# Kernel tuning notes

Hardware: AMD Instinct MI355X
Metric: run time of the kernel (lower is better)

The kernel has to match this reference:

```python
import jax, jax.numpy as jnp
import numpy as np
from jax import lax

DEPTH = 2
HEADS = 8
TEMP = 1.0

def _ln_last(x, g, b, eps=1e-5):
    m = x.mean(-1, keepdims=True)
    v = ((x - m) ** 2).mean(-1, keepdims=True)
    return (x - m) / jnp.sqrt(v + eps) * g + b

def _ln_chan(x, g, b, eps=1e-6):
    # torch custom LayerNorm over channel dim of NCHW, biased var
    m = x.mean(1, keepdims=True)
    v = ((x - m) ** 2).mean(1, keepdims=True)
    return (x - m) / jnp.sqrt(v + eps) * g[None, :, None, None] + b[None, :, None, None]

def _conv3x3(x, w):
    return lax.conv_general_dilated(x, w, (1, 1), ((1, 1), (1, 1)),
                                    dimension_numbers=('NCHW', 'OIHW', 'NCHW'))

def _transformer(x, ln1_g, ln1_b, qkv_w, qkv_b, out_w, out_b, ln2_g, ln2_b,
                 mlp_w1, mlp_b1, mlp_w2, mlp_b2):
    dim = x.shape[-1]
    dh = dim // HEADS
    scale = dh ** -0.5
    for i in range(DEPTH):
        h = _ln_last(x, ln1_g[i], ln1_b[i])
        qkv = h @ qkv_w[i] + qkv_b[i]
        q, k, v = jnp.split(qkv, 3, axis=-1)
        sp = lambda t: t.reshape(t.shape[0], t.shape[1], HEADS, dh).transpose(0, 2, 1, 3)
        q, k, v = sp(q), sp(k), sp(v)
        attn = jax.nn.softmax(jnp.einsum('bhid,bhjd->bhij', q, k) * scale, axis=-1) / TEMP
        o = jnp.einsum('bhij,bhjd->bhid', attn, v).transpose(0, 2, 1, 3).reshape(x.shape)
        x = o @ out_w[i] + out_b[i] + x
        h = _ln_last(x, ln2_g[i], ln2_b[i])
        x = jax.nn.gelu(h @ mlp_w1[i] + mlp_b1[i], approximate=False) @ mlp_w2[i] + mlp_b2[i] + x
    return x

def _tacf(support_feature, query_feature, task_descriptor, ln1_g, ln1_b, qkv_w, qkv_b,
          out_w, out_b, ln2_g, ln2_b, mlp_w1, mlp_b1, mlp_w2, mlp_b2,
          rfm_ln_g, rfm_ln_b, rfm_conv1, rfm_conv2, rfm_conv3, rfm_conv4):
    n, c, h, w = support_feature.shape
    M = task_descriptor.shape[1]
    # descriptor generator: 'n c h w -> 1 (n h w) c', prepend descriptors
    sf = support_feature.transpose(0, 2, 3, 1).reshape(1, n * h * w, c)
    x = jnp.concatenate([task_descriptor, sf], axis=1)
    x = _transformer(x, ln1_g, ln1_b, qkv_w, qkv_b, out_w, out_b, ln2_g, ln2_b,
                     mlp_w1, mlp_b1, mlp_w2, mlp_b2)
    key0 = x[0, :M, :]  # (M, C)

    def region(feat):
        # mean over C of feat[:,None,c,h,w]*key[m,c] == matmul / C
        return jax.nn.sigmoid(jnp.einsum('bchw,mc->bmhw', feat, key0) / feat.shape[1])

    def map_fuse(reg, feat):
        # mean over m of (feat*task + feat) == feat*(mean_m(task)+1)
        return feat * (reg.mean(1, keepdims=True) + 1.0)

    def rfm(x4):
        t = _ln_chan(x4, rfm_ln_g, rfm_ln_b)
        t = jax.nn.relu(_conv3x3(t, rfm_conv1))
        t = jax.nn.relu(_conv3x3(t, rfm_conv2))
        t = jax.nn.relu(_conv3x3(t, rfm_conv3))
        t = _conv3x3(t, rfm_conv4)
        b_, T_, h_, w_ = t.shape
        t = jax.nn.sigmoid(t.reshape(b_, T_, h_ * w_))  # (B,T,HW)
        feat = x4.transpose(0, 2, 3, 1).reshape(b_, h_ * w_, -1)  # (B,HW,C)
        out = jnp.einsum('btp,bpc->btc', t, feat) / (h_ * w_)  # mean over HW
        return out.transpose(0, 2, 1)  # (B,C,T)

    qr = region(query_feature)
    sr = region(support_feature)
    aq = map_fuse(qr, query_feature)
    asp = map_fuse(sr, support_feature)
    return (rfm(asp), rfm(aq))

def setup_inputs() -> dict:
    key = jax.random.key(0)
    ks = jax.random.split(key, 12)
    B_S, B_Q, C, H, W = 25, 75, 128, 10, 10
    M, T, MLP = 16, 32, 512
    rn = lambda k, s, sc=1.0: jax.random.normal(k, s, dtype=jnp.float32) * sc
    return {
        'support_feature': rn(ks[0], (B_S, C, H, W)),
        'query_feature': rn(ks[1], (B_Q, C, H, W)),
        'task_descriptor': rn(ks[2], (1, M, C)),
        'ln1_g': jnp.ones((DEPTH, C), jnp.float32), 'ln1_b': jnp.zeros((DEPTH, C), jnp.float32),
        'qkv_w': rn(ks[3], (DEPTH, C, 3 * C), 0.02), 'qkv_b': jnp.zeros((DEPTH, 3 * C), jnp.float32),
        'out_w': rn(ks[4], (DEPTH, C, C), 0.02), 'out_b': jnp.zeros((DEPTH, C), jnp.float32),
        'ln2_g': jnp.ones((DEPTH, C), jnp.float32), 'ln2_b': jnp.zeros((DEPTH, C), jnp.float32),
        'mlp_w1': rn(ks[5], (DEPTH, C, MLP), 0.02), 'mlp_b1': jnp.zeros((DEPTH, MLP), jnp.float32),
        'mlp_w2': rn(ks[6], (DEPTH, MLP, C), 0.02), 'mlp_b2': jnp.zeros((DEPTH, C), jnp.float32),
        'rfm_ln_g': jnp.ones((C,), jnp.float32), 'rfm_ln_b': jnp.zeros((C,), jnp.float32),
        'rfm_conv1': rn(ks[7], (T, C, 3, 3), 0.05),
        'rfm_conv2': rn(ks[8], (T, T, 3, 3), 0.05),
        'rfm_conv3': rn(ks[9], (T, T, 3, 3), 0.05),
        'rfm_conv4': rn(ks[10], (T, T, 3, 3), 0.05),
    }

def reference(support_feature, query_feature, task_descriptor, ln1_g, ln1_b, qkv_w, qkv_b,
              out_w, out_b, ln2_g, ln2_b, mlp_w1, mlp_b1, mlp_w2, mlp_b2,
              rfm_ln_g, rfm_ln_b, rfm_conv1, rfm_conv2, rfm_conv3, rfm_conv4):
    return _tacf(support_feature, query_feature, task_descriptor, ln1_g, ln1_b, qkv_w, qkv_b,
                 out_w, out_b, ln2_g, ln2_b, mlp_w1, mlp_b1, mlp_w2, mlp_b2,
                 rfm_ln_g, rfm_ln_b, rfm_conv1, rfm_conv2, rfm_conv3, rfm_conv4)
```

## Files before the change

kernel.cpp:

```cpp
#include <hip/hip_runtime.h>
#include <math.h>

#define SEQ 2516
#define SEQP 2520
#define SEQP2 2560
#define CDIM 128

typedef __attribute__((ext_vector_type(8))) short short8;
typedef __attribute__((ext_vector_type(4))) float f32x4;

__device__ __forceinline__ float gelu_exact(float x) {
    return x * 0.5f * (1.0f + erff(x * 0.7071067811865475f));
}
__device__ __forceinline__ float fexp2(float x) { return __builtin_amdgcn_exp2f(x); }
__device__ __forceinline__ short f2bf(float f) {
    unsigned u = __float_as_uint(f);
    unsigned r = 0x7fffu + ((u >> 16) & 1u);
    return (short)((u + r) >> 16);
}
__device__ __forceinline__ short f2bf_trunc(float f) {
    return (short)(__float_as_uint(f) >> 16);
}

__global__ __launch_bounds__(64) void concat_ln_kernel(
    const float* __restrict__ td, const float* __restrict__ sup,
    const float* __restrict__ g, const float* __restrict__ b,
    float* __restrict__ X, float* __restrict__ H) {
    const int row = blockIdx.x;
    const int t = threadIdx.x;
    float x0, x1;
    if (row < 16) {
        x0 = td[row * 128 + t];
        x1 = td[row * 128 + 64 + t];
    } else {
        int r = row - 16;
        int n = r / 100, p = r - n * 100;
        x0 = sup[n * 12800 + t * 100 + p];
        x1 = sup[n * 12800 + (t + 64) * 100 + p];
    }
    X[row * 128 + t] = x0;
    X[row * 128 + 64 + t] = x1;
    float s = x0 + x1;
    for (int off = 32; off > 0; off >>= 1) s += __shfl_down(s, off);
    float mean = __shfl(s, 0) * (1.f / 128.f);
    float d0 = x0 - mean, d1 = x1 - mean;
    float v = d0 * d0 + d1 * d1;
    for (int off = 32; off > 0; off >>= 1) v += __shfl_down(v, off);
    float var = __shfl(v, 0) * (1.f / 128.f);
    float rstd = rsqrtf(var + 1e-5f);
    H[row * 128 + t]      = d0 * rstd * g[t] + b[t];
    H[row * 128 + 64 + t] = d1 * rstd * g[t + 64] + b[t + 64];
}

__global__ __launch_bounds__(256) void qkv_mfma_kernel(
    const float* __restrict__ A, const float* __restrict__ W,
    const float* __restrict__ bias,
    short* __restrict__ Qbf, short* __restrict__ Kbf, short* __restrict__ VTb,
    int q_mt) {
    if (blockIdx.y < 2 && (int)blockIdx.x >= q_mt) return;
    __shared__ __align__(16) short Wt[64 * 136];
    const int t = threadIdx.x;
    const int wave = t >> 6, lane = t & 63;
    const int quad = lane >> 4, c16 = lane & 15;
    const int m0 = blockIdx.x * 64;
    const int n0 = blockIdx.y * 64;
    const float SC = 0.25f * 1.4426950408889634f;
    #pragma unroll
    for (int pass = 0; pass < 4; ++pass) {
        int idx = t + pass * 256;
        int n = idx & 63, kc = idx >> 6;
        short8 wv;
        #pragma unroll
        for (int j = 0; j < 8; ++j)
            wv[j] = f2bf(W[(size_t)(kc * 8 + j) * 384 + n0 + n]);
        *(short8*)&Wt[n * 136 + kc * 8] = wv;
    }
    __syncthreads();
    const int am = m0 + wave * 16 + c16;
    f32x4 acc[4];
    #pragma unroll
    for (int i = 0; i < 4; ++i) acc[i] = (f32x4){0.f, 0.f, 0.f, 0.f};
    #pragma unroll
    for (int kk = 0; kk < 4; ++kk) {
        const float4* ap = (const float4*)(A + (size_t)am * 128 + kk * 32 + quad * 8);
        float4 a0 = ap[0], a1 = ap[1];
        short8 af;
        af[0] = f2bf(a0.x); af[1] = f2bf(a0.y); af[2] = f2bf(a0.z); af[3] = f2bf(a0.w);
        af[4] = f2bf(a1.x); af[5] = f2bf(a1.y); af[6] = f2bf(a1.z); af[7] = f2bf(a1.w);
        #pragma unroll
        for (int ns = 0; ns < 4; ++ns) {
            short8 wf = *(const short8*)&Wt[(ns * 16 + c16) * 136 + kk * 32 + quad * 8];
            acc[ns] = __builtin_amdgcn_mfma_f32_16x16x32_bf16(af, wf, acc[ns], 0, 0, 0);
        }
    }
    const int region = __builtin_amdgcn_readfirstlane(n0 >> 7);
    #pragma unroll
    for (int ns = 0; ns < 4; ++ns) {
        const int n = n0 + ns * 16 + c16;
        float bv = bias[n];
        #pragma unroll
        for (int r = 0; r < 4; ++r) {
            const int row = m0 + wave * 16 + quad * 4 + r;
            float v = acc[ns][r] + bv;
            if (region == 0)      Qbf[(size_t)row * 128 + n] = f2bf(v * SC);
            else if (region == 1) Kbf[(size_t)row * 128 + (n - 128)] = f2bf(v);
            else                  VTb[(size_t)(n - 256) * SEQP2 + row] = f2bf(v);
        }
    }
}

__global__ __launch_bounds__(256) void mlp_fused_kernel(
    const float* __restrict__ A, const float* __restrict__ W1,
    const float* __restrict__ b1, const float* __restrict__ W2,
    float* __restrict__ PARTG) {
    __shared__ __align__(16) short W1t[64 * 136];
    __shared__ __align__(16) short W2t[128 * 72];
    __shared__ __align__(16) short Ct[4 * 16 * 72];
    const int t = threadIdx.x;
    const int wave = t >> 6, lane = t & 63;
    const int quad = lane >> 4, c16 = lane & 15;
    const int m0 = blockIdx.x * 64;
    const int kz = blockIdx.y;
    const int n0 = kz * 64;
    #pragma unroll
    for (int pass = 0; pass < 4; ++pass) {
        int idx = t + pass * 256;
        int n = idx & 63, kc = idx >> 6;
        short8 wv;
        #pragma unroll
        for (int j = 0; j < 8; ++j)
            wv[j] = f2bf(W1[(size_t)(kc * 8 + j) * 512 + n0 + n]);
        *(short8*)&W1t[n * 136 + kc * 8] = wv;
    }
    {
        const int n = t & 127, half = t >> 7;
        #pragma unroll
        for (int c = 0; c < 4; ++c) {
            short8 wv;
            #pragma unroll
            for (int j = 0; j < 8; ++j)
                wv[j] = f2bf(W2[(size_t)(n0 + half * 32 + c * 8 + j) * 128 + n]);
            *(short8*)&W2t[n * 72 + half * 32 + c * 8] = wv;
        }
    }
    __syncthreads();
    const int am = m0 + wave * 16 + c16;
    f32x4 acc1[4];
    #pragma unroll
    for (int i = 0; i < 4; ++i) acc1[i] = (f32x4){0.f, 0.f, 0.f, 0.f};
    #pragma unroll
    for (int kk = 0; kk < 4; ++kk) {
        const float4* ap = (const float4*)(A + (size_t)am * 128 + kk * 32 + quad * 8);
        float4 a0 = ap[0], a1 = ap[1];
        short8 af;
        af[0] = f2bf(a0.x); af[1] = f2bf(a0.y); af[2] = f2bf(a0.z); af[3] = f2bf(a0.w);
        af[4] = f2bf(a1.x); af[5] = f2bf(a1.y); af[6] = f2bf(a1.z); af[7] = f2bf(a1.w);
        #pragma unroll
        for (int ns = 0; ns < 4; ++ns) {
            short8 wf = *(const short8*)&W1t[(ns * 16 + c16) * 136 + kk * 32 + quad * 8];
            acc1[ns] = __builtin_amdgcn_mfma_f32_16x16x32_bf16(af, wf, acc1[ns], 0, 0, 0);
        }
    }
    short* Cw = Ct + wave * 16 * 72;
    #pragma unroll
    for (int ns = 0; ns < 4; ++ns) {
        float bv = b1[n0 + ns * 16 + c16];
        #pragma unroll
        for (int r = 0; r < 4; ++r)
            Cw[(quad * 4 + r) * 72 + ns * 16 + c16] = f2bf(gelu_exact(acc1[ns][r] + bv));
    }
    f32x4 acc2[8];
    #pragma unroll
    for (int i = 0; i < 8; ++i) acc2[i] = (f32x4){0.f, 0.f, 0.f, 0.f};
    #pragma unroll
    for (int kk = 0; kk < 2; ++kk) {
        short8 af2 = *(const short8*)&Cw[c16 * 72 + kk * 32 + quad * 8];
        #pragma unroll
        for (int ns = 0; ns < 8; ++ns) {
            short8 wf = *(const short8*)&W2t[(ns * 16 + c16) * 72 + kk * 32 + quad * 8];
            acc2[ns] = __builtin_amdgcn_mfma_f32_16x16x32_bf16(af2, wf, acc2[ns], 0, 0, 0);
        }
    }
    float* dst = PARTG + (size_t)kz * SEQP2 * 128;
    #pragma unroll
    for (int ns = 0; ns < 8; ++ns) {
        #pragma unroll
        for (int r = 0; r < 4; ++r) {
            const int row = m0 + wave * 16 + quad * 4 + r;
            dst[(size_t)row * 128 + ns * 16 + c16] = acc2[ns][r];
        }
    }
}

__global__ __launch_bounds__(512) void combine_ln_kernel(
    const float* __restrict__ PARTG, const float* __restrict__ bias,
    const float* __restrict__ R, float* __restrict__ C, float* __restrict__ H,
    const float* __restrict__ g, const float* __restrict__ bb, int M) {
    __shared__ float ln[8][130];
    const int t = threadIdx.x;
    const int c = t & 127;
    const int grp = __builtin_amdgcn_readfirstlane(t >> 7);
    const int r0 = blockIdx.x * 8 + grp * 2;
    #pragma unroll
    for (int i = 0; i < 2; ++i) {
        const int row = r0 + i;
        float v = bias[c] + R[(size_t)row * 128 + c];
        #pragma unroll
        for (int kz = 0; kz < 8; ++kz)
            v += PARTG[(size_t)kz * SEQP2 * 128 + (size_t)row * 128 + c];
        ln[grp * 2 + i][c] = v;
        if (row < M) C[(size_t)row * 128 + c] = v;
    }
    __syncthreads();
    const int wv = t >> 6, l = t & 63;
    float x0 = ln[wv][l], x1 = ln[wv][l + 64];
    float s = x0 + x1;
    for (int off = 32; off > 0; off >>= 1) s += __shfl_down(s, off);
    float mean = __shfl(s, 0) * (1.f / 128.f);
    float d0 = x0 - mean, d1 = x1 - mean;
    float vv = d0 * d0 + d1 * d1;
    for (int off = 32; off > 0; off >>= 1) vv += __shfl_down(vv, off);
    float var = __shfl(vv, 0) * (1.f / 128.f);
    float rstd = rsqrtf(var + 1e-5f);
    const int hrow = blockIdx.x * 8 + wv;
    H[(size_t)hrow * 128 + l]      = d0 * rstd * g[l] + bb[l];
    H[(size_t)hrow * 128 + 64 + l] = d1 * rstd * g[l + 64] + bb[l + 64];
}

__global__ __launch_bounds__(512) void proj_merge_ln_kernel(
    const float* __restrict__ PART, const float* __restrict__ W,
    const float* __restrict__ bias, const float* __restrict__ R,
    float* __restrict__ C, float* __restrict__ H,
    const float* __restrict__ g, const float* __restrict__ bb, int M) {
    __shared__ float ln[8][130];
    const int t = threadIdx.x;
    const int c = t & 127;
    const int grp = __builtin_amdgcn_readfirstlane(t >> 7);
    const int r0 = blockIdx.x * 8 + grp * 2;
    float acc0 = 0.f, acc1 = 0.f;
    #pragma unroll
    for (int h = 0; h < 8; ++h) {
        const float* p0a = PART + ((size_t)h * SEQP + r0) * 20;
        const float* p1a = PART + ((size_t)(8 + h) * SEQP + r0) * 20;
        const float* p0b = p0a + 20;
        const float* p1b = p1a + 20;
        float m0 = p0a[16], l0 = p0a[17], m1 = p1a[16], l1 = p1a[17];
        float Ma = fmaxf(m0, m1);
        float w0 = fexp2(m0 - Ma), w1 = fexp2(m1 - Ma);
        float inva = 1.f / fmaf(l0, w0, l1 * w1);
        float c0a = w0 * inva, c1a = w1 * inva;
        m0 = p0b[16]; l0 = p0b[17]; m1 = p1b[16]; l1 = p1b[17];
        float Mb = fmaxf(m0, m1);
        w0 = fexp2(m0 - Mb); w1 = fexp2(m1 - Mb);
        float invb = 1.f / fmaf(l0, w0, l1 * w1);
        float c0b = w0 * invb, c1b = w1 * invb;
        #pragma unroll
        for (int kk = 0; kk < 4; ++kk) {
            const int k0 = h * 16 + kk * 4;
            float w_0 = W[(size_t)(k0 + 0) * 128 + c];
            float w_1 = W[(size_t)(k0 + 1) * 128 + c];
            float w_2 = W[(size_t)(k0 + 2) * 128 + c];
            float w_3 = W[(size_t)(k0 + 3) * 128 + c];
            float4 x0 = *(const float4*)&p0a[kk * 4];
            float4 y0 = *(const float4*)&p1a[kk * 4];
            float4 x1 = *(const float4*)&p0b[kk * 4];
            float4 y1 = *(const float4*)&p1b[kk * 4];
            float a00 = x0.x * c0a + y0.x * c1a;
            float a01 = x0.y * c0a + y0.y * c1a;
            float a02 = x0.z * c0a + y0.z * c1a;
            float a03 = x0.w * c0a + y0.w * c1a;
            float a10 = x1.x * c0b + y1.x * c1b;
            float a11 = x1.y * c0b + y1.y * c1b;
            float a12 = x1.z * c0b + y1.z * c1b;
            float a13 = x1.w * c0b + y1.w * c1b;
            acc0 = fmaf(a00, w_0, acc0); acc0 = fmaf(a01, w_1, acc0);
            acc0 = fmaf(a02, w_2, acc0); acc0 = fmaf(a03, w_3, acc0);
            acc1 = fmaf(a10, w_0, acc1); acc1 = fmaf(a11, w_1, acc1);
            acc1 = fmaf(a12, w_2, acc1); acc1 = fmaf(a13, w_3, acc1);
        }
    }
    float bv = bias[c];
    float v0 = acc0 + bv + R[(size_t)(r0 + 0) * 128 + c];
    float v1 = acc1 + bv + R[(size_t)(r0 + 1) * 128 + c];
    ln[grp * 2 + 0][c] = v0;
    ln[grp * 2 + 1][c] = v1;
    if (r0 + 0 < M) C[(size_t)(r0 + 0) * 128 + c] = v0;
    if (r0 + 1 < M) C[(size_t)(r0 + 1) * 128 + c] = v1;
    __syncthreads();
    const int wv = t >> 6, l = t & 63;
    float x0 = ln[wv][l], x1 = ln[wv][l + 64];
    float s = x0 + x1;
    for (int off = 32; off > 0; off >>= 1) s += __shfl_down(s, off);
    float mean = __shfl(s, 0) * (1.f / 128.f);
    float d0 = x0 - mean, d1 = x1 - mean;
    float vv = d0 * d0 + d1 * d1;
    for (int off = 32; off > 0; off >>= 1) vv += __shfl_down(vv, off);
    float var = __shfl(vv, 0) * (1.f / 128.f);
    float rstd = rsqrtf(var + 1e-5f);
    const int hrow = blockIdx.x * 8 + wv;
    H[(size_t)hrow * 128 + l]      = d0 * rstd * g[l] + bb[l];
    H[(size_t)hrow * 128 + 64 + l] = d1 * rstd * g[l + 64] + bb[l + 64];
}

__global__ __launch_bounds__(128) void attn_kernel(
    const short* __restrict__ Qbf, const short* __restrict__ Kbf,
    const short* __restrict__ VTb, float* __restrict__ PART) {
    __shared__ __align__(16) short sKs[9600];
    short* Ks = sKs;
    short* Vt = sKs + 3072;
    const int t = threadIdx.x;
    const int wave = t >> 6, lane = t & 63;
    const int quad = lane >> 4, c16 = lane & 15;
    short* Pw = sKs + 3072 + 2176 + wave * 16 * 136;
    const int head = blockIdx.y, z = blockIdx.z;
    const int qb = blockIdx.x * 32 + wave * 16;

    short8 qf;
    #pragma unroll
    for (int i = 0; i < 8; ++i) qf[i] = 0;
    if (quad < 2)
        qf = *(const short8*)(Qbf + (size_t)(qb + c16) * 128 + head * 16 + quad * 8);
    f32x4 oacc = {0.f, 0.f, 0.f, 0.f};
    float m_[4] = {-INFINITY, -INFINITY, -INFINITY, -INFINITY};
    float l_[4] = {0.f, 0.f, 0.f, 0.f};

    const int vdim = t >> 3, vseg = t & 7;
    const int tA = z * 10, tB = z ? 20 : 10;
    for (int ti = tA; ti < tB; ++ti) {
        const int tile0 = ti * 128;
        if (ti != tA) __syncthreads();
        {
            const short8* kp = (const short8*)(Kbf + (size_t)(tile0 + t) * 128 + head * 16);
            *(short8*)&Ks[t * 24]     = kp[0];
            *(short8*)&Ks[t * 24 + 8] = kp[1];
            const short8* vp = (const short8*)(VTb + (size_t)(head * 16 + vdim) * SEQP2 + tile0 + vseg * 16);
            *(short8*)&Vt[vdim * 136 + vseg * 16]     = vp[0];
            *(short8*)&Vt[vdim * 136 + vseg * 16 + 8] = vp[1];
        }
        __syncthreads();

        f32x4 sA[4], sB[4];
        #pragma unroll
        for (int st = 0; st < 4; ++st) {
            const int k0 = st * 32;
            short8 kfA, kfB;
            #pragma unroll
            for (int i = 0; i < 8; ++i) { kfA[i] = 0; kfB[i] = 0; }
            if (quad < 2) {
                kfA = *(const short8*)&Ks[(k0 + c16) * 24 + quad * 8];
                kfB = *(const short8*)&Ks[(k0 + 16 + c16) * 24 + quad * 8];
            }
            f32x4 zz = {0.f, 0.f, 0.f, 0.f};
            sA[st] = __builtin_amdgcn_mfma_f32_16x16x32_bf16(qf, kfA, zz, 0, 0, 0);
            sB[st] = __builtin_amdgcn_mfma_f32_16x16x32_bf16(qf, kfB, zz, 0, 0, 0);
            const bool badA = (tile0 + k0 + c16) >= SEQ;
            const bool badB = (tile0 + k0 + 16 + c16) >= SEQ;
            if (badA) { sA[st][0] = -1e30f; sA[st][1] = -1e30f; sA[st][2] = -1e30f; sA[st][3] = -1e30f; }
            if (badB) { sB[st][0] = -1e30f; sB[st][1] = -1e30f; sB[st][2] = -1e30f; sB[st][3] = -1e30f; }
        }
        #pragma unroll
        for (int r = 0; r < 4; ++r) {
            float v = fmaxf(sA[0][r], sB[0][r]);
            #pragma unroll
            for (int st = 1; st < 4; ++st) v = fmaxf(v, fmaxf(sA[st][r], sB[st][r]));
            v = fmaxf(v, __shfl_xor(v, 1));
            v = fmaxf(v, __shfl_xor(v, 2));
            v = fmaxf(v, __shfl_xor(v, 4));
            v = fmaxf(v, __shfl_xor(v, 8));
            float nm = fmaxf(m_[r], v);
            float corr = fexp2(m_[r] - nm);
            m_[r] = nm;
            oacc[r] *= corr;
            l_[r] *= corr;
        }
        #pragma unroll
        for (int st = 0; st < 4; ++st) {
            #pragma unroll
            for (int r = 0; r < 4; ++r) {
                float eA = fexp2(sA[st][r] - m_[r]);
                float eB = fexp2(sB[st][r] - m_[r]);
                l_[r] += eA + eB;
                Pw[(quad * 4 + r) * 136 + st * 32 + c16]      = f2bf_trunc(eA);
                Pw[(quad * 4 + r) * 136 + st * 32 + 16 + c16] = f2bf_trunc(eB);
            }
        }
        #pragma unroll
        for (int st = 0; st < 4; ++st) {
            short8 pf = *(const short8*)&Pw[c16 * 136 + st * 32 + quad * 8];
            short8 vf = *(const short8*)&Vt[c16 * 136 + st * 32 + quad * 8];
            oacc = __builtin_amdgcn_mfma_f32_16x16x32_bf16(pf, vf, oacc, 0, 0, 0);
        }
    }
    #pragma unroll
    for (int r = 0; r < 4; ++r) {
        float lr = l_[r];
        lr += __shfl_xor(lr, 1);
        lr += __shfl_xor(lr, 2);
        lr += __shfl_xor(lr, 4);
        lr += __shfl_xor(lr, 8);
        const int qrow = qb + quad * 4 + r;
        if (qrow < SEQ) {
            float* dst = PART + ((size_t)(z * 8 + head) * SEQP + qrow) * 20;
            dst[c16] = oacc[r];
            if (c16 == 0) { dst[16] = m_[r]; dst[17] = lr; }
        }
    }
}

__global__ __launch_bounds__(256) void region_fuse_stats_kernel(
    const float* __restrict__ sup, const float* __restrict__ qry,
    const float* __restrict__ X, float* __restrict__ fused,
    float* __restrict__ MEAN, float* __restrict__ RSTD) {
    __shared__ float key0[2048];
    __shared__ float rfac[100];
    const int b = blockIdx.x;
    const int t = threadIdx.x;
    const float* feat = (b < 25) ? (sup + (size_t)b * 12800) : (qry + (size_t)(b - 25) * 12800);
    for (int i = t; i < 2048; i += 256) key0[i] = X[i];
    __syncthreads();
    if (t < 100) {
        float dots[16];
        #pragma unroll
        for (int mm = 0; mm < 16; ++mm) dots[mm] = 0.f;
        float s = 0.f, ss = 0.f;
        for (int c = 0; c < 128; ++c) {
            float f = feat[c * 100 + t];
            s += f; ss += f * f;
            #pragma unroll
            for (int mm = 0; mm < 16; ++mm) dots[mm] += f * key0[mm * 128 + c];
        }
        float mean16 = 0.f;
        #pragma unroll
        for (int mm = 0; mm < 16; ++mm) mean16 += 1.f / (1.f + expf(-dots[mm] * (1.f / 128.f)));
        float r = mean16 * (1.f / 16.f) + 1.f;
        rfac[t] = r;
        float mr = s * (1.f / 128.f);
        float vr = ss * (1.f / 128.f) - mr * mr;
        MEAN[b * 128 + t] = mr * r;
        RSTD[b * 128 + t] = rsqrtf(vr * r * r + 1e-6f);
    }
    __syncthreads();
    for (int i = t; i < 12800; i += 256)
        fused[(size_t)b * 12800 + i] = feat[i] * rfac[i % 100];
}

__global__ __launch_bounds__(256) void conv1_split_kernel(
    const float* __restrict__ in, const float* __restrict__ w,
    const float* __restrict__ MEAN, const float* __restrict__ RSTD,
    const float* __restrict__ g, const float* __restrict__ bb,
    float* __restrict__ PARTC) {
    __shared__ float sin_[32 * 144];
    const int b = blockIdx.x;
    const int base_to = blockIdx.y * 8;
    const int cb = blockIdx.z * 32;
    const int t = threadIdx.x;
    const int h = __builtin_amdgcn_readfirstlane(t >> 7);
    const int p = t & 127;
    const int py = p / 10, px = p - py * 10;
    const bool active = p < 100;
    float acc[4] = {0.f, 0.f, 0.f, 0.f};
    for (int i = t; i < 32 * 144; i += 256) {
        int c = i / 144, pos = i - c * 144;
        int y = pos / 12 - 1, x = pos % 12 - 1;
        float v = 0.f;
        if ((unsigned)y < 10u && (unsigned)x < 10u) {
            int pp = y * 10 + x;
            float raw = in[(size_t)b * 12800 + (cb + c) * 100 + pp];
            v = (raw - MEAN[b * 128 + pp]) * RSTD[b * 128 + pp] * g[cb + c] + bb[cb + c];
        }
        sin_[i] = v;
    }
    __syncthreads();
    if (active) {
        const float* wbase = w + ((size_t)(base_to + h * 4) * 128 + cb) * 9;
        for (int c = 0; c < 32; ++c) {
            const float* sp = &sin_[c * 144 + py * 12 + px];
            float pix[9];
            #pragma unroll
            for (int k = 0; k < 9; ++k) pix[k] = sp[(k / 3) * 12 + (k % 3)];
            #pragma unroll
            for (int j = 0; j < 4; ++j) {
                const float* wq = wbase + ((size_t)j * 128 + c) * 9;
                #pragma unroll
                for (int k = 0; k < 9; ++k) acc[j] = fmaf(pix[k], wq[k], acc[j]);
            }
        }
        #pragma unroll
        for (int j = 0; j < 4; ++j)
            PARTC[((size_t)blockIdx.z * 100 + b) * 3200 + (base_to + h * 4 + j) * 100 + p] = acc[j];
    }
}

template<bool RELU, bool COMBINE>
__global__ __launch_bounds__(256) void conv3x3_to4_kernel(
    const float* __restrict__ in, const float* __restrict__ w,
    float* __restrict__ out) {
    __shared__ float sin_[32 * 144];
    const int b = blockIdx.x;
    const int base_to = blockIdx.y * 4;
    const int t = threadIdx.x;
    const int h = __builtin_amdgcn_readfirstlane(t >> 7);
    const int p = t & 127;
    const int py = p / 10, px = p - py * 10;
    const bool active = p < 100;
    float acc[2] = {0.f, 0.f};
    for (int i = t; i < 32 * 144; i += 256) {
        int c = i / 144, pos = i - c * 144;
        int y = pos / 12 - 1, x = pos % 12 - 1;
        float v = 0.f;
        if ((unsigned)y < 10u && (unsigned)x < 10u) {
            if (COMBINE) {
                const size_t base = (size_t)b * 3200 + c * 100 + y * 10 + x;
                v = in[base] + in[base + 320000] + in[base + 640000] + in[base + 960000];
                v = fmaxf(v, 0.f);
            } else {
                v = in[(size_t)b * 3200 + c * 100 + y * 10 + x];
            }
        }
        sin_[i] = v;
    }
    __syncthreads();
    if (active) {
        const float* wbase = w + ((size_t)(base_to + h * 2) * 32) * 9;
        for (int c = 0; c < 32; ++c) {
            const float* sp = &sin_[c * 144 + py * 12 + px];
            float pix[9];
            #pragma unroll
            for (int k = 0; k < 9; ++k) pix[k] = sp[(k / 3) * 12 + (k % 3)];
            #pragma unroll
            for (int j = 0; j < 2; ++j) {
                const float* wq = wbase + ((size_t)j * 32 + c) * 9;
                #pragma unroll
                for (int k = 0; k < 9; ++k) acc[j] = fmaf(pix[k], wq[k], acc[j]);
            }
        }
        #pragma unroll
        for (int j = 0; j < 2; ++j) {
            float v = acc[j];
            if (RELU) v = fmaxf(v, 0.f);
            out[(size_t)b * 3200 + (base_to + h * 2 + j) * 100 + p] = v;
        }
    }
}

__global__ __launch_bounds__(256) void conv4_rfm_kernel(
    const float* __restrict__ in, const float* __restrict__ w,
    const float* __restrict__ fused, float* __restrict__ out) {
    __shared__ float sin_[32 * 144];
    __shared__ float sig[4][104];
    const int b = blockIdx.x;
    const int base_to = blockIdx.y * 4;
    const int t = threadIdx.x;
    const int h = __builtin_amdgcn_readfirstlane(t >> 7);
    const int p = t & 127;
    const int py = p / 10, px = p - py * 10;
    const bool active = p < 100;
    float acc[2] = {0.f, 0.f};
    for (int i = t; i < 32 * 144; i += 256) {
        int c = i / 144, pos = i - c * 144;
        int y = pos / 12 - 1, x = pos % 12 - 1;
        float v = 0.f;
        if ((unsigned)y < 10u && (unsigned)x < 10u)
            v = in[(size_t)b * 3200 + c * 100 + y * 10 + x];
        sin_[i] = v;
    }
    __syncthreads();
    if (active) {
        const float* wbase = w + ((size_t)(base_to + h * 2) * 32) * 9;
        for (int c = 0; c < 32; ++c) {
            const float* sp = &sin_[c * 144 + py * 12 + px];
            float pix[9];
            #pragma unroll
            for (int k = 0; k < 9; ++k) pix[k] = sp[(k / 3) * 12 + (k % 3)];
            #pragma unroll
            for (int j = 0; j < 2; ++j) {
                const float* wq = wbase + ((size_t)j * 32 + c) * 9;
                #pragma unroll
                for (int k = 0; k < 9; ++k) acc[j] = fmaf(pix[k], wq[k], acc[j]);
            }
        }
        sig[h * 2 + 0][p] = 1.f / (1.f + expf(-acc[0]));
        sig[h * 2 + 1][p] = 1.f / (1.f + expf(-acc[1]));
    }
    __syncthreads();
    #pragma unroll
    for (int rep = 0; rep < 2; ++rep) {
        const int o = t + rep * 256;
        const int cc = o >> 2, ttl = o & 3;
        const float* fp = fused + (size_t)b * 12800 + cc * 100;
        float s = 0.f;
        for (int pp = 0; pp < 100; pp += 4) {
            float4 f4 = *(const float4*)&fp[pp];
            s += sig[ttl][pp] * f4.x + sig[ttl][pp + 1] * f4.y
               + sig[ttl][pp + 2] * f4.z + sig[ttl][pp + 3] * f4.w;
        }
        out[(size_t)b * 4096 + cc * 32 + base_to + ttl] = s * 0.01f;
    }
}

extern "C" void kernel_launch(void* const* d_in, const int* in_sizes, int n_in,
                              void* d_out, int out_size, void* d_ws, size_t ws_size,
                              hipStream_t stream) {
    (void)in_sizes; (void)n_in; (void)out_size; (void)ws_size;
    const float* sup    = (const float*)d_in[0];
    const float* qry    = (const float*)d_in[1];
    const float* td     = (const float*)d_in[2];
    const float* ln1_g  = (const float*)d_in[3];
    const float* ln1_b  = (const float*)d_in[4];
    const float* qkv_w  = (const float*)d_in[5];
    const float* qkv_b  = (const float*)d_in[6];
    const float* out_w  = (const float*)d_in[7];
    const float* out_b  = (const float*)d_in[8];
    const float* ln2_g  = (const float*)d_in[9];
    const float* ln2_b  = (const float*)d_in[10];
    const float* mlp_w1 = (const float*)d_in[11];
    const float* mlp_b1 = (const float*)d_in[12];
    const float* mlp_w2 = (const float*)d_in[13];
    const float* mlp_b2 = (const float*)d_in[14];
    const float* rg     = (const float*)d_in[15];
    const float* rb     = (const float*)d_in[16];
    const float* c1     = (const float*)d_in[17];
    const float* c2     = (const float*)d_in[18];
    const float* c3     = (const float*)d_in[19];
    const float* c4     = (const float*)d_in[20];
    float* out = (float*)d_out;

    float* ws   = (float*)d_ws;
    float* X    = ws;
    float* H    = X + 327680;
    float* PARTC= H + 327680;
    float* FUSED= PARTC + 1280000;
    float* MEAN = FUSED + 1280000;
    float* RSTD = MEAN + 12800;
    float* CB1  = RSTD + 12800;
    float* CB2  = CB1 + 320000;
    short* Qbf  = (short*)(CB2 + 320000);
    short* Kbf  = Qbf + 327680;
    short* VTb  = Kbf + 327680;
    float* PARTG= (float*)(VTb + 327680);
    float* PART = PARTG;

    const int SG = (SEQ + 7) / 8;
    const int MT = (SEQ + 63) / 64;

    concat_ln_kernel<<<SEQ, 64, 0, stream>>>(td, sup, ln1_g, ln1_b, X, H);
    for (int i = 0; i < 2; ++i) {
        const int qmt    = (i == 0) ? MT : 1;
        const int atiles = (i == 0) ? (SEQ + 31) / 32 : 1;
        const int sg     = (i == 0) ? SG : 2;
        const int mmt    = (i == 0) ? MT : 1;
        qkv_mfma_kernel<<<dim3(MT, 6), 256, 0, stream>>>(
            H, qkv_w + (size_t)i * 128 * 384, qkv_b + i * 384, Qbf, Kbf, VTb, qmt);
        attn_kernel<<<dim3(atiles, 8, 2), 128, 0, stream>>>(Qbf, Kbf, VTb, PART);
        proj_merge_ln_kernel<<<sg, 512, 0, stream>>>(
            PART, out_w + (size_t)i * 128 * 128, out_b + i * 128, X, X, H,
            ln2_g + i * 128, ln2_b + i * 128, SEQ);
        mlp_fused_kernel<<<dim3(mmt, 8), 256, 0, stream>>>(
            H, mlp_w1 + (size_t)i * 128 * 512, mlp_b1 + i * 512,
            mlp_w2 + (size_t)i * 512 * 128, PARTG);
        const float* ng = (i == 0) ? ln1_g + 128 : ln1_g;
        const float* nb = (i == 0) ? ln1_b + 128 : ln1_b;
        combine_ln_kernel<<<sg, 512, 0, stream>>>(
            PARTG, mlp_b2 + i * 128, X, X, H, ng, nb, SEQ);
    }
    region_fuse_stats_kernel<<<100, 256, 0, stream>>>(sup, qry, X, FUSED, MEAN, RSTD);
    conv1_split_kernel<<<dim3(100, 4, 4), 256, 0, stream>>>(FUSED, c1, MEAN, RSTD, rg, rb, PARTC);
    conv3x3_to4_kernel<true,  true ><<<dim3(100, 8), 256, 0, stream>>>(PARTC, c2, CB2);
    conv3x3_to4_kernel<true,  false><<<dim3(100, 8), 256, 0, stream>>>(CB2, c3, CB1);
    conv4_rfm_kernel<<<dim3(100, 8), 256, 0, stream>>>(CB1, c4, FUSED, out);
}
```

Baseline: 316.6 us.

## Rewrite RFM conv stack as bf16 MFMA implicit-GEMM kernels with channel-last layout

Replaces the scalar FP32 conv path (split-K conv1 with partial sums, per-output-group conv kernels, conv4 with reduction) with one block per sample that runs each 3x3 conv as an implicit GEMM on bf16 MFMA, using channel-last bf16 intermediates. The fused features are stored position-major (FUSEDT) so the final pooling reads coalesced columns. This removes the split-K partial buffers and the extra launches, and moves the conv FLOPs to matrix cores, at the cost of bf16 rounding of the activations and weights. The attention and MLP kernels only change position in the file.

New measurement: 274.6 us. -13.3%, faster.

```diff
diff --git a/kernel.cpp b/kernel.cpp
--- a/kernel.cpp
+++ b/kernel.cpp
@@ -109,122 +109,109 @@
     }
 }
 
-__global__ __launch_bounds__(256) void mlp_fused_kernel(
-    const float* __restrict__ A, const float* __restrict__ W1,
-    const float* __restrict__ b1, const float* __restrict__ W2,
-    float* __restrict__ PARTG) {
-    __shared__ __align__(16) short W1t[64 * 136];
-    __shared__ __align__(16) short W2t[128 * 72];
-    __shared__ __align__(16) short Ct[4 * 16 * 72];
+__global__ __launch_bounds__(128) void attn_kernel(
+    const short* __restrict__ Qbf, const short* __restrict__ Kbf,
+    const short* __restrict__ VTb, float* __restrict__ PART) {
+    __shared__ __align__(16) short sKs[9600];
+    short* Ks = sKs;
+    short* Vt = sKs + 3072;
     const int t = threadIdx.x;
     const int wave = t >> 6, lane = t & 63;
     const int quad = lane >> 4, c16 = lane & 15;
-    const int m0 = blockIdx.x * 64;
-    const int kz = blockIdx.y;
-    const int n0 = kz * 64;
-    #pragma unroll
-    for (int pass = 0; pass < 4; ++pass) {
-        int idx = t + pass * 256;
-        int n = idx & 63, kc = idx >> 6;
-        short8 wv;
-        #pragma unroll
-        for (int j = 0; j < 8; ++j)
-            wv[j] = f2bf(W1[(size_t)(kc * 8 + j) * 512 + n0 + n]);
-        *(short8*)&W1t[n * 136 + kc * 8] = wv;
-    }
-    {
-        const int n = t & 127, half = t >> 7;
-        #pragma unroll
-        for (int c = 0; c < 4; ++c) {
-            short8 wv;
-            #pragma unroll
-            for (int j = 0; j < 8; ++j)
-                wv[j] = f2bf(W2[(size_t)(n0 + half * 32 + c * 8 + j) * 128 + n]);
-            *(short8*)&W2t[n * 72 + half * 32 + c * 8] = wv;
-        }
-    }
-    __syncthreads();
-    const int am = m0 + wave * 16 + c16;
-    f32x4 acc1[4];
-    #pragma unroll
-    for (int i = 0; i < 4; ++i) acc1[i] = (f32x4){0.f, 0.f, 0.f, 0.f};
-    #pragma unroll
-    for (int kk = 0; kk < 4; ++kk) {
-        const float4* ap = (const float4*)(A + (size_t)am * 128 + kk * 32 + quad * 8);
-        float4 a0 = ap[0], a1 = ap[1];
-        short8 af;
-        af[0] = f2bf(a0.x); af[1] = f2bf(a0.y); af[2] = f2bf(a0.z); af[3] = f2bf(a0.w);
-        af[4] = f2bf(a1.x); af[5] = f2bf(a1.y); af[6] = f2bf(a1.z); af[7] = f2bf(a1.w);
-        #pragma unroll
-        for (int ns = 0; ns < 4; ++ns) {
-            short8 wf = *(const short8*)&W1t[(ns * 16 + c16) * 136 + kk * 32 + quad * 8];
-            acc1[ns] = __builtin_amdgcn_mfma_f32_16x16x32_bf16(af, wf, acc1[ns], 0, 0, 0);
-        }
-    }
-    short* Cw = Ct + wave * 16 * 72;
-    #pragma unroll
-    for (int ns = 0; ns < 4; ++ns) {
-        float bv = b1[n0 + ns * 16 + c16];
-        #pragma unroll
-        for (int r = 0; r < 4; ++r)
-            Cw[(quad * 4 + r) * 72 + ns * 16 + c16] = f2bf(gelu_exact(acc1[ns][r] + bv));
-    }
-    f32x4 acc2[8];
-    #pragma unroll
-    for (int i = 0; i < 8; ++i) acc2[i] = (f32x4){0.f, 0.f, 0.f, 0.f};
-    #pragma unroll
-    for (int kk = 0; kk < 2; ++kk) {
-        short8 af2 = *(const short8*)&Cw[c16 * 72 + kk * 32 + quad * 8];
-        #pragma unroll
-        for (int ns = 0; ns < 8; ++ns) {
-            short8 wf = *(const short8*)&W2t[(ns * 16 + c16) * 72 + kk * 32 + quad * 8];
-            acc2[ns] = __builtin_amdgcn_mfma_f32_16x16x32_bf16(af2, wf, acc2[ns], 0, 0, 0);
-        }
-    }
-    float* dst = PARTG + (size_t)kz * SEQP2 * 128;
-    #pragma unroll
-    for (int ns = 0; ns < 8; ++ns) {
+    short* Pw = sKs + 3072 + 2176 + wave * 16 * 136;
+    const int head = blockIdx.y, z = blockIdx.z;
+    const int qb = blockIdx.x * 32 + wave * 16;
+
+    short8 qf;
+    #pragma unroll
+    for (int i = 0; i < 8; ++i) qf[i] = 0;
+    if (quad < 2)
+        qf = *(const short8*)(Qbf + (size_t)(qb + c16) * 128 + head * 16 + quad * 8);
+    f32x4 oacc = {0.f, 0.f, 0.f, 0.f};
+    float m_[4] = {-INFINITY, -INFINITY, -INFINITY, -INFINITY};
+    float l_[4] = {0.f, 0.f, 0.f, 0.f};
+
+    const int vdim = t >> 3, vseg = t & 7;
+    const int tA = z * 10, tB = z ? 20 : 10;
+    for (int ti = tA; ti < tB; ++ti) {
+        const int tile0 = ti * 128;
+        if (ti != tA) __syncthreads();
+        {
+            const short8* kp = (const short8*)(Kbf + (size_t)(tile0 + t) * 128 + head * 16);
+            *(short8*)&Ks[t * 24]     = kp[0];
+            *(short8*)&Ks[t * 24 + 8] = kp[1];
+            const short8* vp = (const short8*)(VTb + (size_t)(head * 16 + vdim) * SEQP2 + tile0 + vseg * 16);
+            *(short8*)&Vt[vdim * 136 + vseg * 16]     = vp[0];
+            *(short8*)&Vt[vdim * 136 + vseg * 16 + 8] = vp[1];
+        }
+        __syncthreads();
+
+        f32x4 sA[4], sB[4];
+        #pragma unroll
+        for (int st = 0; st < 4; ++st) {
+            const int k0 = st * 32;
+            short8 kfA, kfB;
+            #pragma unroll
+            for (int i = 0; i < 8; ++i) { kfA[i] = 0; kfB[i] = 0; }
+            if (quad < 2) {
+                kfA = *(const short8*)&Ks[(k0 + c16) * 24 + quad * 8];
+                kfB = *(const short8*)&Ks[(k0 + 16 + c16) * 24 + quad * 8];
+            }
+            f32x4 zz = {0.f, 0.f, 0.f, 0.f};
+            sA[st] = __builtin_amdgcn_mfma_f32_16x16x32_bf16(qf, kfA, zz, 0, 0, 0);
+            sB[st] = __builtin_amdgcn_mfma_f32_16x16x32_bf16(qf, kfB, zz, 0, 0, 0);
+            const bool badA = (tile0 + k0 + c16) >= SEQ;
+            const bool badB = (tile0 + k0 + 16 + c16) >= SEQ;
+            if (badA) { sA[st][0] = -1e30f; sA[st][1] = -1e30f; sA[st][2] = -1e30f; sA[st][3] = -1e30f; }
+            if (badB) { sB[st][0] = -1e30f; sB[st][1] = -1e30f; sB[st][2] = -1e30f; sB[st][3] = -1e30f; }
+        }
         #pragma unroll
         for (int r = 0; r < 4; ++r) {
-            const int row = m0 + wave * 16 + quad * 4 + r;
-            dst[(size_t)row * 128 + ns * 16 + c16] = acc2[ns][r];
-        }
-    }
-}
-
-__global__ __launch_bounds__(512) void combine_ln_kernel(
-    const float* __restrict__ PARTG, const float* __restrict__ bias,
-    const float* __restrict__ R, float* __restrict__ C, float* __restrict__ H,
-    const float* __restrict__ g, const float* __restrict__ bb, int M) {
-    __shared__ float ln[8][130];
-    const int t = threadIdx.x;
-    const int c = t & 127;
-    const int grp = __builtin_amdgcn_readfirstlane(t >> 7);
-    const int r0 = blockIdx.x * 8 + grp * 2;
-    #pragma unroll
-    for (int i = 0; i < 2; ++i) {
-        const int row = r0 + i;
-        float v = bias[c] + R[(size_t)row * 128 + c];
-        #pragma unroll
-        for (int kz = 0; kz < 8; ++kz)
-            v += PARTG[(size_t)kz * SEQP2 * 128 + (size_t)row * 128 + c];
-        ln[grp * 2 + i][c] = v;
-        if (row < M) C[(size_t)row * 128 + c] = v;
-    }
-    __syncthreads();
-    const int wv = t >> 6, l = t & 63;
-    float x0 = ln[wv][l], x1 = ln[wv][l + 64];
-    float s = x0 + x1;
-    for (int off = 32; off > 0; off >>= 1) s += __shfl_down(s, off);
-    float mean = __shfl(s, 0) * (1.f / 128.f);
-    float d0 = x0 - mean, d1 = x1 - mean;
-    float vv = d0 * d0 + d1 * d1;
-    for (int off = 32; off > 0; off >>= 1) vv += __shfl_down(vv, off);
-    float var = __shfl(vv, 0) * (1.f / 128.f);
-    float rstd = rsqrtf(var + 1e-5f);
-    const int hrow = blockIdx.x * 8 + wv;
-    H[(size_t)hrow * 128 + l]      = d0 * rstd * g[l] + bb[l];
-    H[(size_t)hrow * 128 + 64 + l] = d1 * rstd * g[l + 64] + bb[l + 64];
+            float v = fmaxf(sA[0][r], sB[0][r]);
+            #pragma unroll
+            for (int st = 1; st < 4; ++st) v = fmaxf(v, fmaxf(sA[st][r], sB[st][r]));
+            v = fmaxf(v, __shfl_xor(v, 1));
+            v = fmaxf(v, __shfl_xor(v, 2));
+            v = fmaxf(v, __shfl_xor(v, 4));
+            v = fmaxf(v, __shfl_xor(v, 8));
+            float nm = fmaxf(m_[r], v);
+            float corr = fexp2(m_[r] - nm);
+            m_[r] = nm;
+            oacc[r] *= corr;
+            l_[r] *= corr;
+        }
+        #pragma unroll
+        for (int st = 0; st < 4; ++st) {
+            #pragma unroll
+            for (int r = 0; r < 4; ++r) {
+                float eA = fexp2(sA[st][r] - m_[r]);
+                float eB = fexp2(sB[st][r] - m_[r]);
+                l_[r] += eA + eB;
+                Pw[(quad * 4 + r) * 136 + st * 32 + c16]      = f2bf_trunc(eA);
+                Pw[(quad * 4 + r) * 136 + st * 32 + 16 + c16] = f2bf_trunc(eB);
+            }
+        }
+        #pragma unroll
+        for (int st = 0; st < 4; ++st) {
+            short8 pf = *(const short8*)&Pw[c16 * 136 + st * 32 + quad * 8];
+            short8 vf = *(const short8*)&Vt[c16 * 136 + st * 32 + quad * 8];
+            oacc = __builtin_amdgcn_mfma_f32_16x16x32_bf16(pf, vf, oacc, 0, 0, 0);
+        }
+    }
+    #pragma unroll
+    for (int r = 0; r < 4; ++r) {
+        float lr = l_[r];
+        lr += __shfl_xor(lr, 1);
+        lr += __shfl_xor(lr, 2);
+        lr += __shfl_xor(lr, 4);
+        lr += __shfl_xor(lr, 8);
+        const int qrow = qb + quad * 4 + r;
+        if (qrow < SEQ) {
+            float* dst = PART + ((size_t)(z * 8 + head) * SEQP + qrow) * 20;
+            dst[c16] = oacc[r];
+            if (c16 == 0) { dst[16] = m_[r]; dst[17] = lr; }
+        }
+    }
 }
 
 __global__ __launch_bounds__(512) void proj_merge_ln_kernel(
@@ -302,114 +289,127 @@
     H[(size_t)hrow * 128 + 64 + l] = d1 * rstd * g[l + 64] + bb[l + 64];
 }
 
-__global__ __launch_bounds__(128) void attn_kernel(
-    const short* __restrict__ Qbf, const short* __restrict__ Kbf,
-    const short* __restrict__ VTb, float* __restrict__ PART) {
-    __shared__ __align__(16) short sKs[9600];
-    short* Ks = sKs;
-    short* Vt = sKs + 3072;
+__global__ __launch_bounds__(256) void mlp_fused_kernel(
+    const float* __restrict__ A, const float* __restrict__ W1,
+    const float* __restrict__ b1, const float* __restrict__ W2,
+    float* __restrict__ PARTG) {
+    __shared__ __align__(16) short W1t[64 * 136];
+    __shared__ __align__(16) short W2t[128 * 72];
+    __shared__ __align__(16) short Ct[4 * 16 * 72];
     const int t = threadIdx.x;
     const int wave = t >> 6, lane = t & 63;
     const int quad = lane >> 4, c16 = lane & 15;
-    short* Pw = sKs + 3072 + 2176 + wave * 16 * 136;
-    const int head = blockIdx.y, z = blockIdx.z;
-    const int qb = blockIdx.x * 32 + wave * 16;
-
-    short8 qf;
-    #pragma unroll
-    for (int i = 0; i < 8; ++i) qf[i] = 0;
-    if (quad < 2)
-        qf = *(const short8*)(Qbf + (size_t)(qb + c16) * 128 + head * 16 + quad * 8);
-    f32x4 oacc = {0.f, 0.f, 0.f, 0.f};
-    float m_[4] = {-INFINITY, -INFINITY, -INFINITY, -INFINITY};
-    float l_[4] = {0.f, 0.f, 0.f, 0.f};
-
-    const int vdim = t >> 3, vseg = t & 7;
-    const int tA = z * 10, tB = z ? 20 : 10;
-    for (int ti = tA; ti < tB; ++ti) {
-        const int tile0 = ti * 128;
-        if (ti != tA) __syncthreads();
-        {
-            const short8* kp = (const short8*)(Kbf + (size_t)(tile0 + t) * 128 + head * 16);
-            *(short8*)&Ks[t * 24]     = kp[0];
-            *(short8*)&Ks[t * 24 + 8] = kp[1];
-            const short8* vp = (const short8*)(VTb + (size_t)(head * 16 + vdim) * SEQP2 + tile0 + vseg * 16);
-            *(short8*)&Vt[vdim * 136 + vseg * 16]     = vp[0];
-            *(short8*)&Vt[vdim * 136 + vseg * 16 + 8] = vp[1];
-        }
-        __syncthreads();
-
-        f32x4 sA[4], sB[4];
-        #pragma unroll
-        for (int st = 0; st < 4; ++st) {
-            const int k0 = st * 32;
-            short8 kfA, kfB;
-            #pragma unroll
-            for (int i = 0; i < 8; ++i) { kfA[i] = 0; kfB[i] = 0; }
-            if (quad < 2) {
-                kfA = *(const short8*)&Ks[(k0 + c16) * 24 + quad * 8];
-                kfB = *(const short8*)&Ks[(k0 + 16 + c16) * 24 + quad * 8];
-            }
-            f32x4 zz = {0.f, 0.f, 0.f, 0.f};
-            sA[st] = __builtin_amdgcn_mfma_f32_16x16x32_bf16(qf, kfA, zz, 0, 0, 0);
-            sB[st] = __builtin_amdgcn_mfma_f32_16x16x32_bf16(qf, kfB, zz, 0, 0, 0);
-            const bool badA = (tile0 + k0 + c16) >= SEQ;
-            const bool badB = (tile0 + k0 + 16 + c16) >= SEQ;
-            if (badA) { sA[st][0] = -1e30f; sA[st][1] = -1e30f; sA[st][2] = -1e30f; sA[st][3] = -1e30f; }
-            if (badB) { sB[st][0] = -1e30f; sB[st][1] = -1e30f; sB[st][2] = -1e30f; sB[st][3] = -1e30f; }
-        }
+    const int m0 = blockIdx.x * 64;
+    const int kz = blockIdx.y;
+    const int n0 = kz * 64;
+    #pragma unroll
+    for (int pass = 0; pass < 4; ++pass) {
+        int idx = t + pass * 256;
+        int n = idx & 63, kc = idx >> 6;
+        short8 wv;
+        #pragma unroll
+        for (int j = 0; j < 8; ++j)
+            wv[j] = f2bf(W1[(size_t)(kc * 8 + j) * 512 + n0 + n]);
+        *(short8*)&W1t[n * 136 + kc * 8] = wv;
+    }
+    {
+        const int n = t & 127, half = t >> 7;
+        #pragma unroll
+        for (int c = 0; c < 4; ++c) {
+            short8 wv;
+            #pragma unroll
+            for (int j = 0; j < 8; ++j)
+                wv[j] = f2bf(W2[(size_t)(n0 + half * 32 + c * 8 + j) * 128 + n]);
+            *(short8*)&W2t[n * 72 + half * 32 + c * 8] = wv;
+        }
+    }
+    __syncthreads();
+    const int am = m0 + wave * 16 + c16;
+    f32x4 acc1[4];
+    #pragma unroll
+    for (int i = 0; i < 4; ++i) acc1[i] = (f32x4){0.f, 0.f, 0.f, 0.f};
+    #pragma unroll
+    for (int kk = 0; kk < 4; ++kk) {
+        const float4* ap = (const float4*)(A + (size_t)am * 128 + kk * 32 + quad * 8);
+        float4 a0 = ap[0], a1 = ap[1];
+        short8 af;
+        af[0] = f2bf(a0.x); af[1] = f2bf(a0.y); af[2] = f2bf(a0.z); af[3] = f2bf(a0.w);
+        af[4] = f2bf(a1.x); af[5] = f2bf(a1.y); af[6] = f2bf(a1.z); af[7] = f2bf(a1.w);
+        #pragma unroll
+        for (int ns = 0; ns < 4; ++ns) {
+            short8 wf = *(const short8*)&W1t[(ns * 16 + c16) * 136 + kk * 32 + quad * 8];
+            acc1[ns] = __builtin_amdgcn_mfma_f32_16x16x32_bf16(af, wf, acc1[ns], 0, 0, 0);
+        }
+    }
+    short* Cw = Ct + wave * 16 * 72;
+    #pragma unroll
+    for (int ns = 0; ns < 4; ++ns) {
+        float bv = b1[n0 + ns * 16 + c16];
+        #pragma unroll
+        for (int r = 0; r < 4; ++r)
+            Cw[(quad * 4 + r) * 72 + ns * 16 + c16] = f2bf(gelu_exact(acc1[ns][r] + bv));
+    }
+    f32x4 acc2[8];
+    #pragma unroll
+    for (int i = 0; i < 8; ++i) acc2[i] = (f32x4){0.f, 0.f, 0.f, 0.f};
+    #pragma unroll
+    for (int kk = 0; kk < 2; ++kk) {
+        short8 af2 = *(const short8*)&Cw[c16 * 72 + kk * 32 + quad * 8];
+        #pragma unroll
+        for (int ns = 0; ns < 8; ++ns) {
+            short8 wf = *(const short8*)&W2t[(ns * 16 + c16) * 72 + kk * 32 + quad * 8];
+            acc2[ns] = __builtin_amdgcn_mfma_f32_16x16x32_bf16(af2, wf, acc2[ns], 0, 0, 0);
+        }
+    }
+    float* dst = PARTG + (size_t)kz * SEQP2 * 128;
+    #pragma unroll
+    for (int ns = 0; ns < 8; ++ns) {
         #pragma unroll
         for (int r = 0; r < 4; ++r) {
-            float v = fmaxf(sA[0][r], sB[0][r]);
-            #pragma unroll
-            for (int st = 1; st < 4; ++st) v = fmaxf(v, fmaxf(sA[st][r], sB[st][r]));
-            v = fmaxf(v, __shfl_xor(v, 1));
-            v = fmaxf(v, __shfl_xor(v, 2));
-            v = fmaxf(v, __shfl_xor(v, 4));
-            v = fmaxf(v, __shfl_xor(v, 8));
-            float nm = fmaxf(m_[r], v);
-            float corr = fexp2(m_[r] - nm);
-            m_[r] = nm;
-            oacc[r] *= corr;
-            l_[r] *= corr;
-        }
-        #pragma unroll
-        for (int st = 0; st < 4; ++st) {
-            #pragma unroll
-            for (int r = 0; r < 4; ++r) {
-                float eA = fexp2(sA[st][r] - m_[r]);
-                float eB = fexp2(sB[st][r] - m_[r]);
-                l_[r] += eA + eB;
-                Pw[(quad * 4 + r) * 136 + st * 32 + c16]      = f2bf_trunc(eA);
-                Pw[(quad * 4 + r) * 136 + st * 32 + 16 + c16] = f2bf_trunc(eB);
-            }
-        }
-        #pragma unroll
-        for (int st = 0; st < 4; ++st) {
-            short8 pf = *(const short8*)&Pw[c16 * 136 + st * 32 + quad * 8];
-            short8 vf = *(const short8*)&Vt[c16 * 136 + st * 32 + quad * 8];
-            oacc = __builtin_amdgcn_mfma_f32_16x16x32_bf16(pf, vf, oacc, 0, 0, 0);
-        }
-    }
-    #pragma unroll
-    for (int r = 0; r < 4; ++r) {
-        float lr = l_[r];
-        lr += __shfl_xor(lr, 1);
-        lr += __shfl_xor(lr, 2);
-        lr += __shfl_xor(lr, 4);
-        lr += __shfl_xor(lr, 8);
-        const int qrow = qb + quad * 4 + r;
-        if (qrow < SEQ) {
-            float* dst = PART + ((size_t)(z * 8 + head) * SEQP + qrow) * 20;
-            dst[c16] = oacc[r];
-            if (c16 == 0) { dst[16] = m_[r]; dst[17] = lr; }
-        }
-    }
+            const int row = m0 + wave * 16 + quad * 4 + r;
+            dst[(size_t)row * 128 + ns * 16 + c16] = acc2[ns][r];
+        }
+    }
+}
+
+__global__ __launch_bounds__(512) void combine_ln_kernel(
+    const float* __restrict__ PARTG, const float* __restrict__ bias,
+    const float* __restrict__ R, float* __restrict__ C, float* __restrict__ H,
+    const float* __restrict__ g, const float* __restrict__ bb, int M) {
+    __shared__ float ln[8][130];
+    const int t = threadIdx.x;
+    const int c = t & 127;
+    const int grp = __builtin_amdgcn_readfirstlane(t >> 7);
+    const int r0 = blockIdx.x * 8 + grp * 2;
+    #pragma unroll
+    for (int i = 0; i < 2; ++i) {
+        const int row = r0 + i;
+        float v = bias[c] + R[(size_t)row * 128 + c];
+        #pragma unroll
+        for (int kz = 0; kz < 8; ++kz)
+            v += PARTG[(size_t)kz * SEQP2 * 128 + (size_t)row * 128 + c];
+        ln[grp * 2 + i][c] = v;
+        if (row < M) C[(size_t)row * 128 + c] = v;
+    }
+    __syncthreads();
+    const int wv = t >> 6, l = t & 63;
+    float x0 = ln[wv][l], x1 = ln[wv][l + 64];
+    float s = x0 + x1;
+    for (int off = 32; off > 0; off >>= 1) s += __shfl_down(s, off);
+    float mean = __shfl(s, 0) * (1.f / 128.f);
+    float d0 = x0 - mean, d1 = x1 - mean;
+    float vv = d0 * d0 + d1 * d1;
+    for (int off = 32; off > 0; off >>= 1) vv += __shfl_down(vv, off);
+    float var = __shfl(vv, 0) * (1.f / 128.f);
+    float rstd = rsqrtf(var + 1e-5f);
+    const int hrow = blockIdx.x * 8 + wv;
+    H[(size_t)hrow * 128 + l]      = d0 * rstd * g[l] + bb[l];
+    H[(size_t)hrow * 128 + 64 + l] = d1 * rstd * g[l + 64] + bb[l + 64];
 }
 
 __global__ __launch_bounds__(256) void region_fuse_stats_kernel(
     const float* __restrict__ sup, const float* __restrict__ qry,
-    const float* __restrict__ X, float* __restrict__ fused,
+    const float* __restrict__ X, float* __restrict__ FUSEDT,
     float* __restrict__ MEAN, float* __restrict__ RSTD) {
     __shared__ float key0[2048];
     __shared__ float rfac[100];
@@ -440,162 +440,225 @@
         RSTD[b * 128 + t] = rsqrtf(vr * r * r + 1e-6f);
     }
     __syncthreads();
-    for (int i = t; i < 12800; i += 256)
-        fused[(size_t)b * 12800 + i] = feat[i] * rfac[i % 100];
-}
-
-__global__ __launch_bounds__(256) void conv1_split_kernel(
-    const float* __restrict__ in, const float* __restrict__ w,
-    const float* __restrict__ MEAN, const float* __restrict__ RSTD,
-    const float* __restrict__ g, const float* __restrict__ bb,
-    float* __restrict__ PARTC) {
-    __shared__ float sin_[32 * 144];
+    for (int i = t; i < 12800; i += 256) {
+        int p = i >> 7, c = i & 127;
+        FUSEDT[(size_t)b * 12800 + i] = feat[c * 100 + p] * rfac[p];
+    }
+}
+
+__global__ __launch_bounds__(256) void conv1_mfma_kernel(
+    const float* __restrict__ FUSEDT, const float* __restrict__ MEAN,
+    const float* __restrict__ RSTD, const float* __restrict__ g,
+    const float* __restrict__ bb, const float* __restrict__ w,
+    short* __restrict__ C1) {
+    __shared__ __align__(16) short inT[144 * 136];
+    __shared__ __align__(16) short Wt[32 * 136];
     const int b = blockIdx.x;
-    const int base_to = blockIdx.y * 8;
-    const int cb = blockIdx.z * 32;
-    const int t = threadIdx.x;
-    const int h = __builtin_amdgcn_readfirstlane(t >> 7);
-    const int p = t & 127;
-    const int py = p / 10, px = p - py * 10;
-    const bool active = p < 100;
-    float acc[4] = {0.f, 0.f, 0.f, 0.f};
-    for (int i = t; i < 32 * 144; i += 256) {
-        int c = i / 144, pos = i - c * 144;
-        int y = pos / 12 - 1, x = pos % 12 - 1;
-        float v = 0.f;
-        if ((unsigned)y < 10u && (unsigned)x < 10u) {
-            int pp = y * 10 + x;
-            float raw = in[(size_t)b * 12800 + (cb + c) * 100 + pp];
-            v = (raw - MEAN[b * 128 + pp]) * RSTD[b * 128 + pp] * g[cb + c] + bb[cb + c];
-        }
-        sin_[i] = v;
-    }
-    __syncthreads();
-    if (active) {
-        const float* wbase = w + ((size_t)(base_to + h * 4) * 128 + cb) * 9;
-        for (int c = 0; c < 32; ++c) {
-            const float* sp = &sin_[c * 144 + py * 12 + px];
-            float pix[9];
-            #pragma unroll
-            for (int k = 0; k < 9; ++k) pix[k] = sp[(k / 3) * 12 + (k % 3)];
-            #pragma unroll
-            for (int j = 0; j < 4; ++j) {
-                const float* wq = wbase + ((size_t)j * 128 + c) * 9;
-                #pragma unroll
-                for (int k = 0; k < 9; ++k) acc[j] = fmaf(pix[k], wq[k], acc[j]);
-            }
-        }
-        #pragma unroll
-        for (int j = 0; j < 4; ++j)
-            PARTC[((size_t)blockIdx.z * 100 + b) * 3200 + (base_to + h * 4 + j) * 100 + p] = acc[j];
-    }
-}
-
-template<bool RELU, bool COMBINE>
-__global__ __launch_bounds__(256) void conv3x3_to4_kernel(
-    const float* __restrict__ in, const float* __restrict__ w,
-    float* __restrict__ out) {
-    __shared__ float sin_[32 * 144];
+    const int t = threadIdx.x;
+    const int wave = t >> 6, lane = t & 63;
+    const int quad = lane >> 4, c16 = lane & 15;
+    for (int idx = t; idx < 2304; idx += 256) {
+        int pos = idx >> 4, cg = idx & 15;
+        int yy = pos / 12, xx = pos - yy * 12;
+        short8 sv;
+        if (yy >= 1 && yy <= 10 && xx >= 1 && xx <= 10) {
+            int pp = (yy - 1) * 10 + (xx - 1);
+            const float4* fp = (const float4*)(FUSEDT + (size_t)b * 12800 + pp * 128 + cg * 8);
+            float4 f0 = fp[0], f1 = fp[1];
+            float mn = MEAN[b * 128 + pp], rs = RSTD[b * 128 + pp];
+            float vals[8] = {f0.x, f0.y, f0.z, f0.w, f1.x, f1.y, f1.z, f1.w};
+            #pragma unroll
+            for (int j = 0; j < 8; ++j)
+                sv[j] = f2bf((vals[j] - mn) * rs * g[cg * 8 + j] + bb[cg * 8 + j]);
+        } else {
+            #pragma unroll
+            for (int j = 0; j < 8; ++j) sv[j] = 0;
+        }
+        *(short8*)&inT[pos * 136 + cg * 8] = sv;
+    }
+    const int m0 = wave * 32 + c16;
+    const int m1 = m0 + 16;
+    const int mc0 = (m0 < 100) ? m0 : 99, mc1 = (m1 < 100) ? m1 : 99;
+    const int base0 = (mc0 / 10) * 12 + (mc0 % 10);
+    const int base1 = (mc1 / 10) * 12 + (mc1 % 10);
+    f32x4 a00 = {0.f,0.f,0.f,0.f}, a01 = {0.f,0.f,0.f,0.f};
+    f32x4 a10 = {0.f,0.f,0.f,0.f}, a11 = {0.f,0.f,0.f,0.f};
+    for (int j = 0; j < 9; ++j) {
+        __syncthreads();
+        for (int i = t; i < 4096; i += 256) {
+            int co = i >> 7, cin = i & 127;
+            Wt[co * 136 + cin] = f2bf(w[(size_t)(co * 128 + cin) * 9 + j]);
+        }
+        __syncthreads();
+        const int offj = (j / 3) * 12 + (j % 3);
+        #pragma unroll
+        for (int kk = 0; kk < 4; ++kk) {
+            short8 af0 = *(const short8*)&inT[(base0 + offj) * 136 + kk * 32 + quad * 8];
+            short8 af1 = *(const short8*)&inT[(base1 + offj) * 136 + kk * 32 + quad * 8];
+            short8 bf0 = *(const short8*)&Wt[c16 * 136 + kk * 32 + quad * 8];
+            short8 bf1 = *(const short8*)&Wt[(16 + c16) * 136 + kk * 32 + quad * 8];
+            a00 = __builtin_amdgcn_mfma_f32_16x16x32_bf16(af0, bf0, a00, 0, 0, 0);
+            a01 = __builtin_amdgcn_mfma_f32_16x16x32_bf16(af0, bf1, a01, 0, 0, 0);
+            a10 = __builtin_amdgcn_mfma_f32_16x16x32_bf16(af1, bf0, a10, 0, 0, 0);
+            a11 = __builtin_amdgcn_mfma_f32_16x16x32_bf16(af1, bf1, a11, 0, 0, 0);
+        }
+    }
+    #pragma unroll
+    for (int r = 0; r < 4; ++r) {
+        const int p0 = wave * 32 + quad * 4 + r;
+        const int p1 = p0 + 16;
+        if (p0 < 100) {
+            C1[((size_t)b * 100 + p0) * 32 + c16]      = f2bf(fmaxf(a00[r], 0.f));
+            C1[((size_t)b * 100 + p0) * 32 + 16 + c16] = f2bf(fmaxf(a01[r], 0.f));
+        }
+        if (p1 < 100) {
+            C1[((size_t)b * 100 + p1) * 32 + c16]      = f2bf(fmaxf(a10[r], 0.f));
+            C1[((size_t)b * 100 + p1) * 32 + 16 + c16] = f2bf(fmaxf(a11[r], 0.f));
+        }
+    }
+}
+
+__global__ __launch_bounds__(256) void conv33_mfma_kernel(
+    const short* __restrict__ Cin_, const float* __restrict__ w,
+    short* __restrict__ Cout) {
+    __shared__ __align__(16) short inT[144 * 40];
+    __shared__ __align__(16) short Wt[9 * 32 * 40];
     const int b = blockIdx.x;
-    const int base_to = blockIdx.y * 4;
-    const int t = threadIdx.x;
-    const int h = __builtin_amdgcn_readfirstlane(t >> 7);
-    const int p = t & 127;
-    const int py = p / 10, px = p - py * 10;
-    const bool active = p < 100;
-    float acc[2] = {0.f, 0.f};
-    for (int i = t; i < 32 * 144; i += 256) {
-        int c = i / 144, pos = i - c * 144;
-        int y = pos / 12 - 1, x = pos % 12 - 1;
-        float v = 0.f;
-        if ((unsigned)y < 10u && (unsigned)x < 10u) {
-            if (COMBINE) {
-                const size_t base = (size_t)b * 3200 + c * 100 + y * 10 + x;
-                v = in[base] + in[base + 320000] + in[base + 640000] + in[base + 960000];
-                v = fmaxf(v, 0.f);
-            } else {
-                v = in[(size_t)b * 3200 + c * 100 + y * 10 + x];
-            }
-        }
-        sin_[i] = v;
-    }
-    __syncthreads();
-    if (active) {
-        const float* wbase = w + ((size_t)(base_to + h * 2) * 32) * 9;
-        for (int c = 0; c < 32; ++c) {
-            const float* sp = &sin_[c * 144 + py * 12 + px];
-            float pix[9];
-            #pragma unroll
-            for (int k = 0; k < 9; ++k) pix[k] = sp[(k / 3) * 12 + (k % 3)];
-            #pragma unroll
-            for (int j = 0; j < 2; ++j) {
-                const float* wq = wbase + ((size_t)j * 32 + c) * 9;
-                #pragma unroll
-                for (int k = 0; k < 9; ++k) acc[j] = fmaf(pix[k], wq[k], acc[j]);
-            }
-        }
-        #pragma unroll
-        for (int j = 0; j < 2; ++j) {
-            float v = acc[j];
-            if (RELU) v = fmaxf(v, 0.f);
-            out[(size_t)b * 3200 + (base_to + h * 2 + j) * 100 + p] = v;
-        }
-    }
-}
-
-__global__ __launch_bounds__(256) void conv4_rfm_kernel(
-    const float* __restrict__ in, const float* __restrict__ w,
-    const float* __restrict__ fused, float* __restrict__ out) {
-    __shared__ float sin_[32 * 144];
-    __shared__ float sig[4][104];
+    const int t = threadIdx.x;
+    const int wave = t >> 6, lane = t & 63;
+    const int quad = lane >> 4, c16 = lane & 15;
+    for (int i = t; i < 9216; i += 256) {
+        int j = i / 1024, rem = i - j * 1024;
+        int co = rem >> 5, ch = rem & 31;
+        Wt[j * 1280 + co * 40 + ch] = f2bf(w[(size_t)co * 288 + ch * 9 + j]);
+    }
+    for (int idx = t; idx < 288; idx += 256) {
+        int pos = idx >> 1, half = idx & 1;
+        int yy = pos / 12, xx = pos - yy * 12;
+        short8 s0, s1;
+        if (yy >= 1 && yy <= 10 && xx >= 1 && xx <= 10) {
+            int pp = (yy - 1) * 10 + (xx - 1);
+            const short8* sp = (const short8*)(Cin_ + ((size_t)b * 100 + pp) * 32 + half * 16);
+            s0 = sp[0]; s1 = sp[1];
+        } else {
+            #pragma unroll
+            for (int j = 0; j < 8; ++j) { s0[j] = 0; s1[j] = 0; }
+        }
+        *(short8*)&inT[pos * 40 + half * 16]     = s0;
+        *(short8*)&inT[pos * 40 + half * 16 + 8] = s1;
+    }
+    __syncthreads();
+    const int m0 = wave * 32 + c16;
+    const int m1 = m0 + 16;
+    const int mc0 = (m0 < 100) ? m0 : 99, mc1 = (m1 < 100) ? m1 : 99;
+    const int base0 = (mc0 / 10) * 12 + (mc0 % 10);
+    const int base1 = (mc1 / 10) * 12 + (mc1 % 10);
+    f32x4 a00 = {0.f,0.f,0.f,0.f}, a01 = {0.f,0.f,0.f,0.f};
+    f32x4 a10 = {0.f,0.f,0.f,0.f}, a11 = {0.f,0.f,0.f,0.f};
+    #pragma unroll
+    for (int j = 0; j < 9; ++j) {
+        const int offj = (j / 3) * 12 + (j % 3);
+        short8 af0 = *(const short8*)&inT[(base0 + offj) * 40 + quad * 8];
+        short8 af1 = *(const short8*)&inT[(base1 + offj) * 40 + quad * 8];
+        short8 bf0 = *(const short8*)&Wt[j * 1280 + c16 * 40 + quad * 8];
+        short8 bf1 = *(const short8*)&Wt[j * 1280 + (16 + c16) * 40 + quad * 8];
+        a00 = __builtin_amdgcn_mfma_f32_16x16x32_bf16(af0, bf0, a00, 0, 0, 0);
+        a01 = __builtin_amdgcn_mfma_f32_16x16x32_bf16(af0, bf1, a01, 0, 0, 0);
+        a10 = __builtin_amdgcn_mfma_f32_16x16x32_bf16(af1, bf0, a10, 0, 0, 0);
+        a11 = __builtin_amdgcn_mfma_f32_16x16x32_bf16(af1, bf1, a11, 0, 0, 0);
+    }
+    #pragma unroll
+    for (int r = 0; r < 4; ++r) {
+        const int p0 = wave * 32 + quad * 4 + r;
+        const int p1 = p0 + 16;
+        if (p0 < 100) {
+            Cout[((size_t)b * 100 + p0) * 32 + c16]      = f2bf(fmaxf(a00[r], 0.f));
+            Cout[((size_t)b * 100 + p0) * 32 + 16 + c16] = f2bf(fmaxf(a01[r], 0.f));
+        }
+        if (p1 < 100) {
+            Cout[((size_t)b * 100 + p1) * 32 + c16]      = f2bf(fmaxf(a10[r], 0.f));
+            Cout[((size_t)b * 100 + p1) * 32 + 16 + c16] = f2bf(fmaxf(a11[r], 0.f));
+        }
+    }
+}
+
+__global__ __launch_bounds__(256) void conv4_pool_kernel(
+    const short* __restrict__ C3, const float* __restrict__ w,
+    const float* __restrict__ FUSEDT, float* __restrict__ out) {
+    __shared__ __align__(16) short inT[144 * 40];
+    __shared__ __align__(16) short Wt[9 * 32 * 40];
+    __shared__ float sig[32 * 104];
     const int b = blockIdx.x;
-    const int base_to = blockIdx.y * 4;
-    const int t = threadIdx.x;
-    const int h = __builtin_amdgcn_readfirstlane(t >> 7);
-    const int p = t & 127;
-    const int py = p / 10, px = p - py * 10;
-    const bool active = p < 100;
-    float acc[2] = {0.f, 0.f};
-    for (int i = t; i < 32 * 144; i += 256) {
-        int c = i / 144, pos = i - c * 144;
-        int y = pos / 12 - 1, x = pos % 12 - 1;
-        float v = 0.f;
-        if ((unsigned)y < 10u && (unsigned)x < 10u)
-            v = in[(size_t)b * 3200 + c * 100 + y * 10 + x];
-        sin_[i] = v;
-    }
-    __syncthreads();
-    if (active) {
-        const float* wbase = w + ((size_t)(base_to + h * 2) * 32) * 9;
-        for (int c = 0; c < 32; ++c) {
-            const float* sp = &sin_[c * 144 + py * 12 + px];
-            float pix[9];
-            #pragma unroll
-            for (int k = 0; k < 9; ++k) pix[k] = sp[(k / 3) * 12 + (k % 3)];
-            #pragma unroll
-            for (int j = 0; j < 2; ++j) {
-                const float* wq = wbase + ((size_t)j * 32 + c) * 9;
-                #pragma unroll
-                for (int k = 0; k < 9; ++k) acc[j] = fmaf(pix[k], wq[k], acc[j]);
-            }
-        }
-        sig[h * 2 + 0][p] = 1.f / (1.f + expf(-acc[0]));
-        sig[h * 2 + 1][p] = 1.f / (1.f + expf(-acc[1]));
-    }
-    __syncthreads();
-    #pragma unroll
-    for (int rep = 0; rep < 2; ++rep) {
-        const int o = t + rep * 256;
-        const int cc = o >> 2, ttl = o & 3;
-        const float* fp = fused + (size_t)b * 12800 + cc * 100;
-        float s = 0.f;
-        for (int pp = 0; pp < 100; pp += 4) {
-            float4 f4 = *(const float4*)&fp[pp];
-            s += sig[ttl][pp] * f4.x + sig[ttl][pp + 1] * f4.y
-               + sig[ttl][pp + 2] * f4.z + sig[ttl][pp + 3] * f4.w;
-        }
-        out[(size_t)b * 4096 + cc * 32 + base_to + ttl] = s * 0.01f;
-    }
+    const int t = threadIdx.x;
+    const int wave = t >> 6, lane = t & 63;
+    const int quad = lane >> 4, c16 = lane & 15;
+    for (int i = t; i < 9216; i += 256) {
+        int j = i / 1024, rem = i - j * 1024;
+        int co = rem >> 5, ch = rem & 31;
+        Wt[j * 1280 + co * 40 + ch] = f2bf(w[(size_t)co * 288 + ch * 9 + j]);
+    }
+    for (int idx = t; idx < 288; idx += 256) {
+        int pos = idx >> 1, half = idx & 1;
+        int yy = pos / 12, xx = pos - yy * 12;
+        short8 s0, s1;
+        if (yy >= 1 && yy <= 10 && xx >= 1 && xx <= 10) {
+            int pp = (yy - 1) * 10 + (xx - 1);
+            const short8* sp = (const short8*)(C3 + ((size_t)b * 100 + pp) * 32 + half * 16);
+            s0 = sp[0]; s1 = sp[1];
+        } else {
+            #pragma unroll
+            for (int j = 0; j < 8; ++j) { s0[j] = 0; s1[j] = 0; }
+        }
+        *(short8*)&inT[pos * 40 + half * 16]     = s0;
+        *(short8*)&inT[pos * 40 + half * 16 + 8] = s1;
+    }
+    __syncthreads();
+    const int m0 = wave * 32 + c16;
+    const int m1 = m0 + 16;
+    const int mc0 = (m0 < 100) ? m0 : 99, mc1 = (m1 < 100) ? m1 : 99;
+    const int base0 = (mc0 / 10) * 12 + (mc0 % 10);
+    const int base1 = (mc1 / 10) * 12 + (mc1 % 10);
+    f32x4 a00 = {0.f,0.f,0.f,0.f}, a01 = {0.f,0.f,0.f,0.f};
+    f32x4 a10 = {0.f,0.f,0.f,0.f}, a11 = {0.f,0.f,0.f,0.f};
+    #pragma unroll
+    for (int j = 0; j < 9; ++j) {
+        const int offj = (j / 3) * 12 + (j % 3);
+        short8 af0 = *(const short8*)&inT[(base0 + offj) * 40 + quad * 8];
+        short8 af1 = *(const short8*)&inT[(base1 + offj) * 40 + quad * 8];
+        short8 bf0 = *(const short8*)&Wt[j * 1280 + c16 * 40 + quad * 8];
+        short8 bf1 = *(const short8*)&Wt[j * 1280 + (16 + c16) * 40 + quad * 8];
+        a00 = __builtin_amdgcn_mfma_f32_16x16x32_bf16(af0, bf0, a00, 0, 0, 0);
+        a01 = __builtin_amdgcn_mfma_f32_16x16x32_bf16(af0, bf1, a01, 0, 0, 0);
+        a10 = __builtin_amdgcn_mfma_f32_16x16x32_bf16(af1, bf0, a10, 0, 0, 0);
+        a11 = __builtin_amdgcn_mfma_f32_16x16x32_bf16(af1, bf1, a11, 0, 0, 0);
+    }
+    #pragma unroll
+    for (int r = 0; r < 4; ++r) {
+        const int p0 = wave * 32 + quad * 4 + r;
+        const int p1 = p0 + 16;
+        if (p0 < 100) {
+            sig[(c16)      * 104 + p0] = 1.f / (1.f + expf(-a00[r]));
+            sig[(16 + c16) * 104 + p0] = 1.f / (1.f + expf(-a01[r]));
+        }
+        if (p1 < 100) {
+            sig[(c16)      * 104 + p1] = 1.f / (1.f + expf(-a10[r]));
+            sig[(16 + c16) * 104 + p1] = 1.f / (1.f + expf(-a11[r]));
+        }
+    }
+    __syncthreads();
+    const int cc = t & 127, h = t >> 7;
+    float accv[16];
+    #pragma unroll
+    for (int k = 0; k < 16; ++k) accv[k] = 0.f;
+    for (int p = 0; p < 100; ++p) {
+        float f = FUSEDT[(size_t)b * 12800 + p * 128 + cc];
+        #pragma unroll
+        for (int k = 0; k < 16; ++k)
+            accv[k] = fmaf(sig[(h + 2 * k) * 104 + p], f, accv[k]);
+    }
+    #pragma unroll
+    for (int k = 0; k < 16; ++k)
+        out[(size_t)b * 4096 + cc * 32 + (h + 2 * k)] = accv[k] * 0.01f;
 }
 
 extern "C" void kernel_launch(void* const* d_in, const int* in_sizes, int n_in,
@@ -625,20 +688,20 @@
     const float* c4     = (const float*)d_in[20];
     float* out = (float*)d_out;
 
-    float* ws   = (float*)d_ws;
-    float* X    = ws;
-    float* H    = X + 327680;
-    float* PARTC= H + 327680;
-    float* FUSED= PARTC + 1280000;
-    float* MEAN = FUSED + 1280000;
-    float* RSTD = MEAN + 12800;
-    float* CB1  = RSTD + 12800;
-    float* CB2  = CB1 + 320000;
-    short* Qbf  = (short*)(CB2 + 320000);
-    short* Kbf  = Qbf + 327680;
-    short* VTb  = Kbf + 327680;
-    float* PARTG= (float*)(VTb + 327680);
-    float* PART = PARTG;
+    float* ws     = (float*)d_ws;
+    float* X      = ws;
+    float* H      = X + 327680;
+    float* FUSEDT = H + 327680;
+    float* MEAN   = FUSEDT + 1280000;
+    float* RSTD   = MEAN + 12800;
+    short* Qbf    = (short*)(RSTD + 12800);
+    short* Kbf    = Qbf + 327680;
+    short* VTb    = Kbf + 327680;
+    short* C1     = VTb + 327680;
+    short* C2     = C1 + 320000;
+    short* C3     = C2 + 320000;
+    float* PARTG  = (float*)(C3 + 320000);
+    float* PART   = PARTG;
 
     const int SG = (SEQ + 7) / 8;
     const int MT = (SEQ + 63) / 64;
@@ -663,9 +726,9 @@
         combine_ln_kernel<<<sg, 512, 0, stream>>>(
             PARTG, mlp_b2 + i * 128, X, X, H, ng, nb, SEQ);
     }
-    region_fuse_stats_kernel<<<100, 256, 0, stream>>>(sup, qry, X, FUSED, MEAN, RSTD);
-    conv1_split_kernel<<<dim3(100, 4, 4), 256, 0, stream>>>(FUSED, c1, MEAN, RSTD, rg, rb, PARTC);
-    conv3x3_to4_kernel<true,  true ><<<dim3(100, 8), 256, 0, stream>>>(PARTC, c2, CB2);
-    conv3x3_to4_kernel<true,  false><<<dim3(100, 8), 256, 0, stream>>>(CB2, c3, CB1);
-    conv4_rfm_kernel<<<dim3(100, 8), 256, 0, stream>>>(CB1, c4, FUSED, out);
-}
+    region_fuse_stats_kernel<<<100, 256, 0, stream>>>(sup, qry, X, FUSEDT, MEAN, RSTD);
+    conv1_mfma_kernel<<<100, 256, 0, stream>>>(FUSEDT, MEAN, RSTD, rg, rb, c1, C1);
+    conv33_mfma_kernel<<<100, 256, 0, stream>>>(C1, c2, C2);
+    conv33_mfma_kernel<<<100, 256, 0, stream>>>(C2, c3, C3);
+    conv4_pool_kernel<<<100, 256, 0, stream>>>(C3, c4, FUSEDT, out);
+}
```
